# Optimization experiments

Measured on AMD Instinct MI355X. Metric: run time of the kernel, lower is better.

Reference implementation:

```python
import jax, jax.numpy as jnp
import numpy as np

N_VERTICES = 1_000_000
N_EDGES = 16_000_000


def setup_inputs() -> dict:
    key = jax.random.key(0)
    k1, k2, k3, k4 = jax.random.split(key, 4)
    # vertex_attr columns: [A_ii, b_i, x_i]; keep A_ii away from 0 for stable division
    A_ii = jax.random.uniform(k1, (N_VERTICES,), jnp.float32, 1.0, 2.0)
    b_i = jax.random.normal(k2, (N_VERTICES,), jnp.float32)
    x_i = jnp.zeros((N_VERTICES,), jnp.float32)
    vertex_attr = jnp.stack([A_ii, b_i, x_i], axis=1)  # [N, 3]
    # edge_attr columns: [A_ij, c_ij] (c_ij is overwritten on first iteration)
    A_ij = jax.random.normal(k3, (N_EDGES,), jnp.float32) * 0.01
    edge_attr = jnp.stack([A_ij, jnp.zeros_like(A_ij)], axis=1)  # [E, 2]
    edgeij_pair = jax.random.randint(k4, (2, N_EDGES), 0, N_VERTICES, jnp.int64)
    g = jnp.array([0.666], jnp.float32)  # Jacobi damping weight w
    return {"n_iters": 10, "vertex_attr": vertex_attr, "edgeij_pair": edgeij_pair,
            "edge_attr": edge_attr, "g": g}


def reference(n_iters, vertex_attr, edgeij_pair, edge_attr, g):
    # MetaLayer convention: row, col = edge_index; vattr_j = x[col]; scatter to row.
    row = edgeij_pair[0]
    col = edgeij_pair[1]
    A_ii = vertex_attr[:, 0]          # [N]
    b_i = vertex_attr[:, 1]           # [N]
    x0 = vertex_attr[:, 2]            # [N]
    A_ij = edge_attr[:, 0]            # [E]
    w = g[0]
    n = A_ii.shape[0]

    def step(x, _):
        # EdgeUpdate: c_ij = A_ij * x_j ; aggregation: cbar_i = sum_j c_ij
        c_ij = A_ij * x[col]                                     # [E]
        cbar = jax.ops.segment_sum(c_ij, row, num_segments=n)    # [N]
        # VertexUpdate: x <- x + w * (b - cbar) / A_ii
        x_new = x + w * (b_i - cbar) / A_ii
        return x_new, None

    x, _ = jax.lax.scan(step, x0, None, length=n_iters)
    return x.reshape(-1, 1)
```

## Files before the change

kernel.cpp:

```cpp
#include <hip/hip_runtime.h>
#include <hip/hip_fp16.h>

static constexpr int BLK  = 256;
static constexpr int B1   = 256;
static constexpr int BLKW = 1024;

__global__ void detect_kernel(const unsigned long long* __restrict__ rc,
                              int* __restrict__ flag) {
    if (blockIdx.x == 0 && threadIdx.x == 0) {
        int is64 = 1;
        for (int i = 0; i < 8; ++i)
            if (rc[i] >= (1ull << 20)) is64 = 0;
        *flag = is64;
    }
}

__global__ void hist1_kernel(const void* __restrict__ rcv,
                             const int* __restrict__ flag,
                             unsigned int* __restrict__ hist, int ne, int nb) {
    __shared__ unsigned int lh[1024];
    const int b = blockIdx.x;
    const int chunk = (ne + B1 - 1) / B1;
    const int s = b * chunk, e = min(ne, s + chunk);
    for (int i = threadIdx.x; i < 1024; i += BLKW) lh[i] = 0u;
    __syncthreads();
    const int is64 = *flag;
    const unsigned long long* r64 = (const unsigned long long*)rcv;
    const unsigned int*       r32 = (const unsigned int*)rcv;
    for (int i = s + threadIdx.x; i < e; i += BLKW) {
        unsigned int row = is64 ? (unsigned int)r64[i] : r32[i];
        atomicAdd(&lh[row >> 10], 1u);
    }
    __syncthreads();
    for (int i = threadIdx.x; i < nb; i += BLKW)
        hist[(size_t)i * B1 + b] = lh[i];
}

__global__ void scan1_kernel(unsigned int* __restrict__ data,
                             unsigned int* __restrict__ part, int n) {
    __shared__ unsigned int s[BLK];
    int t = threadIdx.x;
    int i = blockIdx.x * BLK + t;
    unsigned int v = (i < n) ? data[i] : 0u;
    s[t] = v;
    __syncthreads();
    for (int off = 1; off < BLK; off <<= 1) {
        unsigned int u = (t >= off) ? s[t - off] : 0u;
        __syncthreads();
        s[t] += u;
        __syncthreads();
    }
    if (i < n) data[i] = s[t] - v;
    if (t == BLK - 1) part[blockIdx.x] = s[t];
}

__global__ void scan2_kernel(unsigned int* __restrict__ part, int np) {
    __shared__ unsigned int s[BLK];
    __shared__ unsigned int carry_s;
    int t = threadIdx.x;
    if (t == 0) carry_s = 0u;
    __syncthreads();
    for (int base = 0; base < np; base += BLK) {
        int i = base + t;
        unsigned int v = (i < np) ? part[i] : 0u;
        s[t] = v;
        __syncthreads();
        for (int off = 1; off < BLK; off <<= 1) {
            unsigned int u = (t >= off) ? s[t - off] : 0u;
            __syncthreads();
            s[t] += u;
            __syncthreads();
        }
        unsigned int carry = carry_s;
        if (i < np) part[i] = s[t] - v + carry;
        __syncthreads();
        if (t == BLK - 1) carry_s = carry + s[t];
        __syncthreads();
    }
}

__global__ void scan3_kernel(unsigned int* __restrict__ data,
                             const unsigned int* __restrict__ part, int n) {
    int i = blockIdx.x * BLK + threadIdx.x;
    if (i < n) data[i] += part[blockIdx.x];
}

__global__ void scatter1_kernel(const void* __restrict__ rcv,
                                const float2* __restrict__ eattr,
                                const int* __restrict__ flag,
                                const unsigned int* __restrict__ base,
                                unsigned long long* __restrict__ edges,
                                int ne, int nb) {
    __shared__ unsigned int cur[1024];
    const int b = blockIdx.x;
    const int chunk = (ne + B1 - 1) / B1;
    const int s = b * chunk, e = min(ne, s + chunk);
    for (int i = threadIdx.x; i < nb; i += BLKW)
        cur[i] = base[(size_t)i * B1 + b];
    __syncthreads();
    const int is64 = *flag;
    const unsigned long long* r64 = (const unsigned long long*)rcv;
    const unsigned int*       r32 = (const unsigned int*)rcv;
    for (int i = s + threadIdx.x; i < e; i += BLKW) {
        unsigned long long row, col;
        if (is64) { row = r64[i]; col = r64[(size_t)ne + i]; }
        else      { row = r32[i]; col = r32[(size_t)ne + i]; }
        float a = eattr[i].x;
        unsigned short h = __half_as_ushort(__float2half(a));
        unsigned long long q = (row << 44) | (col << 24) | (unsigned long long)h;
        unsigned int pos = atomicAdd(&cur[(unsigned int)(row >> 10)], 1u);
        edges[pos] = q;
    }
}

__global__ void vprep_kernel(const float* __restrict__ vattr,
                             const float* __restrict__ g,
                             float2* __restrict__ vp,
                             float* __restrict__ x0, int nv) {
    int i = blockIdx.x * BLK + threadIdx.x;
    if (i >= nv) return;
    float A = vattr[3 * i + 0];
    float b = vattr[3 * i + 1];
    float x = vattr[3 * i + 2];
    float w = g[0];
    vp[i] = make_float2(w * b / A, w / A);
    x0[i] = x;
}

__global__ void iter_kernel(const unsigned int* __restrict__ bbase,
                            const unsigned long long* __restrict__ edges,
                            const float2* __restrict__ vp,
                            const float* __restrict__ xin,
                            float* __restrict__ xout,
                            int nv, int ne, int nb) {
    __shared__ float acc[1024];
    const int b = blockIdx.x;
    const int t = threadIdx.x;
    for (int i = t; i < 1024; i += BLK) acc[i] = 0.0f;
    __syncthreads();
    const unsigned int s = bbase[(size_t)b * B1];
    const unsigned int e = (b == nb - 1) ? (unsigned int)ne
                                         : bbase[(size_t)(b + 1) * B1];
    #pragma unroll 4
    for (unsigned int j = s + t; j < e; j += BLK) {
        unsigned long long q = edges[j];
        float a = __half2float(__ushort_as_half((unsigned short)(q & 0xFFFFu)));
        unsigned int col = (unsigned int)(q >> 24) & 0xFFFFFu;
        unsigned int rlo = (unsigned int)(q >> 44) & 1023u;
        atomicAdd(&acc[rlo], a * xin[col]);
    }
    __syncthreads();
    const int r0 = b << 10;
    for (int i = t; i < 1024; i += BLK) {
        int r = r0 + i;
        if (r < nv) {
            float2 qv = vp[r];
            xout[r] = xin[r] + qv.x - qv.y * acc[i];
        }
    }
}

extern "C" void kernel_launch(void* const* d_in, const int* in_sizes, int n_in,
                              void* d_out, int out_size, void* d_ws, size_t ws_size,
                              hipStream_t stream) {
    const float* vattr = (const float*)d_in[1];
    const void*  eij   = (const void*)d_in[2];
    const float* eattr = (const float*)d_in[3];
    const float* g     = (const float*)d_in[4];
    const int nv = in_sizes[1] / 3;
    const int ne = in_sizes[3] / 2;
    const int n_iters = 10;
    const int nb = (nv + 1023) >> 10;
    const int nh = nb * B1;

    char* ws = (char*)d_ws;
    size_t off = 0;
    auto alloc = [&](size_t bytes) -> void* {
        void* p = ws + off;
        off = (off + bytes + 255) & ~(size_t)255;
        return p;
    };
    unsigned long long* edges = (unsigned long long*)alloc((size_t)ne * 8);
    unsigned int* hist = (unsigned int*)alloc((size_t)nh * 4);
    unsigned int* part = (unsigned int*)alloc(((size_t)(nh + BLK - 1) / BLK) * 4);
    float2* vp = (float2*)alloc((size_t)nv * 8);
    float*  xa = (float*) alloc((size_t)nv * 4);
    float*  xb = (float*) alloc((size_t)nv * 4);
    int*  flag = (int*)   alloc(256);

    const int vblocks = (nv + BLK - 1) / BLK;
    const int sblocks = (nh + BLK - 1) / BLK;

    detect_kernel<<<1, 64, 0, stream>>>((const unsigned long long*)eij, flag);
    hist1_kernel<<<B1, BLKW, 0, stream>>>(eij, flag, hist, ne, nb);
    scan1_kernel<<<sblocks, BLK, 0, stream>>>(hist, part, nh);
    scan2_kernel<<<1, BLK, 0, stream>>>(part, sblocks);
    scan3_kernel<<<sblocks, BLK, 0, stream>>>(hist, part, nh);
    scatter1_kernel<<<B1, BLKW, 0, stream>>>(eij, (const float2*)eattr, flag,
                                             hist, edges, ne, nb);
    vprep_kernel<<<vblocks, BLK, 0, stream>>>(vattr, g, vp, xa, nv);

    float* xin  = xa;
    float* xout = xb;
    for (int it = 0; it < n_iters; ++it) {
        float* dst = (it == n_iters - 1) ? (float*)d_out : xout;
        iter_kernel<<<nb, BLK, 0, stream>>>(hist, edges, vp, xin, dst,
                                            nv, ne, nb);
        float* t = xin; xin = dst; xout = t;
    }
}
```

Measured before the change: 1.406 ms.

## Halve row-bucket size, unroll edge loop by 8 with nontemporal loads

```diff
diff --git a/kernel.cpp b/kernel.cpp
--- a/kernel.cpp
+++ b/kernel.cpp
@@ -4,6 +4,9 @@
 static constexpr int BLK  = 256;
 static constexpr int B1   = 256;
 static constexpr int BLKW = 1024;
+static constexpr int RSH  = 9;
+static constexpr int RMSK = 511;
+static constexpr int NBMAX = 2048;
 
 __global__ void detect_kernel(const unsigned long long* __restrict__ rc,
                               int* __restrict__ flag) {
@@ -18,18 +21,18 @@
 __global__ void hist1_kernel(const void* __restrict__ rcv,
                              const int* __restrict__ flag,
                              unsigned int* __restrict__ hist, int ne, int nb) {
-    __shared__ unsigned int lh[1024];
+    __shared__ unsigned int lh[NBMAX];
     const int b = blockIdx.x;
     const int chunk = (ne + B1 - 1) / B1;
     const int s = b * chunk, e = min(ne, s + chunk);
-    for (int i = threadIdx.x; i < 1024; i += BLKW) lh[i] = 0u;
+    for (int i = threadIdx.x; i < NBMAX; i += BLKW) lh[i] = 0u;
     __syncthreads();
     const int is64 = *flag;
     const unsigned long long* r64 = (const unsigned long long*)rcv;
     const unsigned int*       r32 = (const unsigned int*)rcv;
     for (int i = s + threadIdx.x; i < e; i += BLKW) {
         unsigned int row = is64 ? (unsigned int)r64[i] : r32[i];
-        atomicAdd(&lh[row >> 10], 1u);
+        atomicAdd(&lh[row >> RSH], 1u);
     }
     __syncthreads();
     for (int i = threadIdx.x; i < nb; i += BLKW)
@@ -91,7 +94,7 @@
                                 const unsigned int* __restrict__ base,
                                 unsigned long long* __restrict__ edges,
                                 int ne, int nb) {
-    __shared__ unsigned int cur[1024];
+    __shared__ unsigned int cur[NBMAX];
     const int b = blockIdx.x;
     const int chunk = (ne + B1 - 1) / B1;
     const int s = b * chunk, e = min(ne, s + chunk);
@@ -108,7 +111,7 @@
         float a = eattr[i].x;
         unsigned short h = __half_as_ushort(__float2half(a));
         unsigned long long q = (row << 44) | (col << 24) | (unsigned long long)h;
-        unsigned int pos = atomicAdd(&cur[(unsigned int)(row >> 10)], 1u);
+        unsigned int pos = atomicAdd(&cur[(unsigned int)(row >> RSH)], 1u);
         edges[pos] = q;
     }
 }
@@ -127,35 +130,59 @@
     x0[i] = x;
 }
 
+__device__ __forceinline__ void edge_accum(unsigned long long q,
+                                           const float* __restrict__ xin,
+                                           float* acc) {
+    float a = __half2float(__ushort_as_half((unsigned short)(q & 0xFFFFu)));
+    unsigned int col = (unsigned int)(q >> 24) & 0xFFFFFu;
+    unsigned int rlo = (unsigned int)(q >> 44) & RMSK;
+    atomicAdd(&acc[rlo], a * xin[col]);
+}
+
 __global__ void iter_kernel(const unsigned int* __restrict__ bbase,
                             const unsigned long long* __restrict__ edges,
                             const float2* __restrict__ vp,
                             const float* __restrict__ xin,
                             float* __restrict__ xout,
                             int nv, int ne, int nb) {
-    __shared__ float acc[1024];
+    __shared__ float acc[512];
     const int b = blockIdx.x;
     const int t = threadIdx.x;
-    for (int i = t; i < 1024; i += BLK) acc[i] = 0.0f;
+    for (int i = t; i < 512; i += BLK) acc[i] = 0.0f;
     __syncthreads();
     const unsigned int s = bbase[(size_t)b * B1];
     const unsigned int e = (b == nb - 1) ? (unsigned int)ne
                                          : bbase[(size_t)(b + 1) * B1];
-    #pragma unroll 4
-    for (unsigned int j = s + t; j < e; j += BLK) {
-        unsigned long long q = edges[j];
-        float a = __half2float(__ushort_as_half((unsigned short)(q & 0xFFFFu)));
-        unsigned int col = (unsigned int)(q >> 24) & 0xFFFFFu;
-        unsigned int rlo = (unsigned int)(q >> 44) & 1023u;
-        atomicAdd(&acc[rlo], a * xin[col]);
-    }
-    __syncthreads();
-    const int r0 = b << 10;
-    for (int i = t; i < 1024; i += BLK) {
+    unsigned int j = s + t;
+    for (; j + 7u * BLK < e; j += 8u * BLK) {
+        unsigned long long q0 = __builtin_nontemporal_load(&edges[j + 0u * BLK]);
+        unsigned long long q1 = __builtin_nontemporal_load(&edges[j + 1u * BLK]);
+        unsigned long long q2 = __builtin_nontemporal_load(&edges[j + 2u * BLK]);
+        unsigned long long q3 = __builtin_nontemporal_load(&edges[j + 3u * BLK]);
+        unsigned long long q4 = __builtin_nontemporal_load(&edges[j + 4u * BLK]);
+        unsigned long long q5 = __builtin_nontemporal_load(&edges[j + 5u * BLK]);
+        unsigned long long q6 = __builtin_nontemporal_load(&edges[j + 6u * BLK]);
+        unsigned long long q7 = __builtin_nontemporal_load(&edges[j + 7u * BLK]);
+        edge_accum(q0, xin, acc);
+        edge_accum(q1, xin, acc);
+        edge_accum(q2, xin, acc);
+        edge_accum(q3, xin, acc);
+        edge_accum(q4, xin, acc);
+        edge_accum(q5, xin, acc);
+        edge_accum(q6, xin, acc);
+        edge_accum(q7, xin, acc);
+    }
+    for (; j < e; j += BLK) {
+        unsigned long long q = __builtin_nontemporal_load(&edges[j]);
+        edge_accum(q, xin, acc);
+    }
+    __syncthreads();
+    const int r0 = b << RSH;
+    for (int i = t; i < 512; i += BLK) {
         int r = r0 + i;
         if (r < nv) {
             float2 qv = vp[r];
-            xout[r] = xin[r] + qv.x - qv.y * acc[i];
+            __builtin_nontemporal_store(xin[r] + qv.x - qv.y * acc[i], &xout[r]);
         }
     }
 }
@@ -170,7 +197,7 @@
     const int nv = in_sizes[1] / 3;
     const int ne = in_sizes[3] / 2;
     const int n_iters = 10;
-    const int nb = (nv + 1023) >> 10;
+    const int nb = (nv + RMSK) >> RSH;
     const int nh = nb * B1;
 
     char* ws = (char*)d_ws;
```

New measurement: 1.512 ms. +7.6%, slower.

## Sort edges by column within larger row buckets and split accumulation

Applied to the files above, without the earlier changes.

```diff
diff --git a/kernel.cpp b/kernel.cpp
--- a/kernel.cpp
+++ b/kernel.cpp
@@ -4,9 +4,14 @@
 static constexpr int BLK  = 256;
 static constexpr int B1   = 256;
 static constexpr int BLKW = 1024;
-
-__global__ void detect_kernel(const unsigned long long* __restrict__ rc,
-                              int* __restrict__ flag) {
+static constexpr int RSH  = 13;
+static constexpr int RPB  = 8192;
+static constexpr int RMSK = 8191;
+static constexpr int NBMAX = 128;
+
+typedef unsigned long long ull;
+
+__global__ void detect_kernel(const ull* __restrict__ rc, int* __restrict__ flag) {
     if (blockIdx.x == 0 && threadIdx.x == 0) {
         int is64 = 1;
         for (int i = 0; i < 8; ++i)
@@ -18,18 +23,18 @@
 __global__ void hist1_kernel(const void* __restrict__ rcv,
                              const int* __restrict__ flag,
                              unsigned int* __restrict__ hist, int ne, int nb) {
-    __shared__ unsigned int lh[1024];
+    __shared__ unsigned int lh[NBMAX];
     const int b = blockIdx.x;
     const int chunk = (ne + B1 - 1) / B1;
     const int s = b * chunk, e = min(ne, s + chunk);
-    for (int i = threadIdx.x; i < 1024; i += BLKW) lh[i] = 0u;
+    for (int i = threadIdx.x; i < NBMAX; i += BLKW) lh[i] = 0u;
     __syncthreads();
     const int is64 = *flag;
-    const unsigned long long* r64 = (const unsigned long long*)rcv;
-    const unsigned int*       r32 = (const unsigned int*)rcv;
+    const ull*          r64 = (const ull*)rcv;
+    const unsigned int* r32 = (const unsigned int*)rcv;
     for (int i = s + threadIdx.x; i < e; i += BLKW) {
         unsigned int row = is64 ? (unsigned int)r64[i] : r32[i];
-        atomicAdd(&lh[row >> 10], 1u);
+        atomicAdd(&lh[row >> RSH], 1u);
     }
     __syncthreads();
     for (int i = threadIdx.x; i < nb; i += BLKW)
@@ -89,9 +94,8 @@
                                 const float2* __restrict__ eattr,
                                 const int* __restrict__ flag,
                                 const unsigned int* __restrict__ base,
-                                unsigned long long* __restrict__ edges,
-                                int ne, int nb) {
-    __shared__ unsigned int cur[1024];
+                                ull* __restrict__ edges, int ne, int nb) {
+    __shared__ unsigned int cur[NBMAX];
     const int b = blockIdx.x;
     const int chunk = (ne + B1 - 1) / B1;
     const int s = b * chunk, e = min(ne, s + chunk);
@@ -99,17 +103,53 @@
         cur[i] = base[(size_t)i * B1 + b];
     __syncthreads();
     const int is64 = *flag;
-    const unsigned long long* r64 = (const unsigned long long*)rcv;
-    const unsigned int*       r32 = (const unsigned int*)rcv;
+    const ull*          r64 = (const ull*)rcv;
+    const unsigned int* r32 = (const unsigned int*)rcv;
     for (int i = s + threadIdx.x; i < e; i += BLKW) {
-        unsigned long long row, col;
+        ull row, col;
         if (is64) { row = r64[i]; col = r64[(size_t)ne + i]; }
         else      { row = r32[i]; col = r32[(size_t)ne + i]; }
         float a = eattr[i].x;
         unsigned short h = __half_as_ushort(__float2half(a));
-        unsigned long long q = (row << 44) | (col << 24) | (unsigned long long)h;
-        unsigned int pos = atomicAdd(&cur[(unsigned int)(row >> 10)], 1u);
+        ull q = (row << 44) | (col << 24) | (ull)h;
+        unsigned int pos = atomicAdd(&cur[(unsigned int)(row >> RSH)], 1u);
         edges[pos] = q;
+    }
+}
+
+__global__ void colsort_kernel(const ull* __restrict__ edges,
+                               const unsigned int* __restrict__ base,
+                               ull* __restrict__ edges2,
+                               unsigned int* __restrict__ mid, int ne, int nb) {
+    __shared__ unsigned int bins[1024];
+    __shared__ unsigned int cur[1024];
+    const int b = blockIdx.x;
+    const int t = threadIdx.x;
+    const unsigned int s = base[(size_t)b * B1];
+    const unsigned int e = (b == nb - 1) ? (unsigned int)ne
+                                         : base[(size_t)(b + 1) * B1];
+    bins[t] = 0u;
+    __syncthreads();
+    for (unsigned int j = s + t; j < e; j += BLKW) {
+        ull q = edges[j];
+        atomicAdd(&bins[(unsigned int)(q >> 34) & 1023u], 1u);
+    }
+    __syncthreads();
+    unsigned int v = bins[t];
+    for (int off = 1; off < 1024; off <<= 1) {
+        unsigned int u = (t >= off) ? bins[t - off] : 0u;
+        __syncthreads();
+        bins[t] += u;
+        __syncthreads();
+    }
+    unsigned int excl = bins[t] - v;
+    cur[t] = excl;
+    if (t == 512) mid[b] = s + excl;
+    __syncthreads();
+    for (unsigned int j = s + t; j < e; j += BLKW) {
+        ull q = edges[j];
+        unsigned int pos = atomicAdd(&cur[(unsigned int)(q >> 34) & 1023u], 1u);
+        edges2[s + pos] = q;
     }
 }
 
@@ -127,37 +167,51 @@
     x0[i] = x;
 }
 
-__global__ void iter_kernel(const unsigned int* __restrict__ bbase,
-                            const unsigned long long* __restrict__ edges,
-                            const float2* __restrict__ vp,
-                            const float* __restrict__ xin,
-                            float* __restrict__ xout,
-                            int nv, int ne, int nb) {
-    __shared__ float acc[1024];
-    const int b = blockIdx.x;
+__global__ __launch_bounds__(BLKW)
+void iter_kernel(const unsigned int* __restrict__ base,
+                 const unsigned int* __restrict__ mid,
+                 const ull* __restrict__ edges2,
+                 const float* __restrict__ xin,
+                 float* __restrict__ p0, float* __restrict__ p1,
+                 int ne, int nb) {
+    __shared__ float acc[RPB];
+    const int blk = blockIdx.x;
+    const int b = blk >> 1, half = blk & 1;
     const int t = threadIdx.x;
-    for (int i = t; i < 1024; i += BLK) acc[i] = 0.0f;
-    __syncthreads();
-    const unsigned int s = bbase[(size_t)b * B1];
-    const unsigned int e = (b == nb - 1) ? (unsigned int)ne
-                                         : bbase[(size_t)(b + 1) * B1];
+    #pragma unroll
+    for (int i = t; i < RPB; i += BLKW) acc[i] = 0.0f;
+    __syncthreads();
+    const unsigned int s0 = base[(size_t)b * B1];
+    const unsigned int e0 = (b == nb - 1) ? (unsigned int)ne
+                                          : base[(size_t)(b + 1) * B1];
+    const unsigned int m = mid[b];
+    const unsigned int s = half ? m : s0;
+    const unsigned int e = half ? e0 : m;
     #pragma unroll 4
-    for (unsigned int j = s + t; j < e; j += BLK) {
-        unsigned long long q = edges[j];
+    for (unsigned int j = s + t; j < e; j += BLKW) {
+        ull q = edges2[j];
         float a = __half2float(__ushort_as_half((unsigned short)(q & 0xFFFFu)));
         unsigned int col = (unsigned int)(q >> 24) & 0xFFFFFu;
-        unsigned int rlo = (unsigned int)(q >> 44) & 1023u;
-        atomicAdd(&acc[rlo], a * xin[col]);
-    }
-    __syncthreads();
-    const int r0 = b << 10;
-    for (int i = t; i < 1024; i += BLK) {
-        int r = r0 + i;
-        if (r < nv) {
-            float2 qv = vp[r];
-            xout[r] = xin[r] + qv.x - qv.y * acc[i];
-        }
-    }
+        unsigned int r   = (unsigned int)(q >> 44) & RMSK;
+        atomicAdd(&acc[r], a * xin[col]);
+    }
+    __syncthreads();
+    float* p = half ? p1 : p0;
+    const size_t r0 = (size_t)b << RSH;
+    #pragma unroll
+    for (int i = t; i < RPB; i += BLKW) p[r0 + i] = acc[i];
+}
+
+__global__ void merge_kernel(const float* __restrict__ p0,
+                             const float* __restrict__ p1,
+                             const float2* __restrict__ vp,
+                             const float* __restrict__ xin,
+                             float* __restrict__ xout, int nv) {
+    int i = blockIdx.x * BLK + threadIdx.x;
+    if (i >= nv) return;
+    float c = p0[i] + p1[i];
+    float2 q = vp[i];
+    xout[i] = xin[i] + q.x - q.y * c;
 }
 
 extern "C" void kernel_launch(void* const* d_in, const int* in_sizes, int n_in,
@@ -170,8 +224,9 @@
     const int nv = in_sizes[1] / 3;
     const int ne = in_sizes[3] / 2;
     const int n_iters = 10;
-    const int nb = (nv + 1023) >> 10;
+    const int nb = (nv + RMSK) >> RSH;
     const int nh = nb * B1;
+    const int nprows = nb << RSH;
 
     char* ws = (char*)d_ws;
     size_t off = 0;
@@ -180,9 +235,13 @@
         off = (off + bytes + 255) & ~(size_t)255;
         return p;
     };
-    unsigned long long* edges = (unsigned long long*)alloc((size_t)ne * 8);
+    ull* edges  = (ull*)alloc((size_t)ne * 8);
+    ull* edges2 = (ull*)alloc((size_t)ne * 8);
     unsigned int* hist = (unsigned int*)alloc((size_t)nh * 4);
     unsigned int* part = (unsigned int*)alloc(((size_t)(nh + BLK - 1) / BLK) * 4);
+    unsigned int* mid  = (unsigned int*)alloc((size_t)nb * 4);
+    float* p0 = (float*)alloc((size_t)nprows * 4);
+    float* p1 = (float*)alloc((size_t)nprows * 4);
     float2* vp = (float2*)alloc((size_t)nv * 8);
     float*  xa = (float*) alloc((size_t)nv * 4);
     float*  xb = (float*) alloc((size_t)nv * 4);
@@ -191,21 +250,23 @@
     const int vblocks = (nv + BLK - 1) / BLK;
     const int sblocks = (nh + BLK - 1) / BLK;
 
-    detect_kernel<<<1, 64, 0, stream>>>((const unsigned long long*)eij, flag);
+    detect_kernel<<<1, 64, 0, stream>>>((const ull*)eij, flag);
     hist1_kernel<<<B1, BLKW, 0, stream>>>(eij, flag, hist, ne, nb);
     scan1_kernel<<<sblocks, BLK, 0, stream>>>(hist, part, nh);
     scan2_kernel<<<1, BLK, 0, stream>>>(part, sblocks);
     scan3_kernel<<<sblocks, BLK, 0, stream>>>(hist, part, nh);
     scatter1_kernel<<<B1, BLKW, 0, stream>>>(eij, (const float2*)eattr, flag,
                                              hist, edges, ne, nb);
+    colsort_kernel<<<nb, BLKW, 0, stream>>>(edges, hist, edges2, mid, ne, nb);
     vprep_kernel<<<vblocks, BLK, 0, stream>>>(vattr, g, vp, xa, nv);
 
     float* xin  = xa;
     float* xout = xb;
     for (int it = 0; it < n_iters; ++it) {
+        iter_kernel<<<2 * nb, BLKW, 0, stream>>>(hist, mid, edges2, xin,
+                                                 p0, p1, ne, nb);
         float* dst = (it == n_iters - 1) ? (float*)d_out : xout;
-        iter_kernel<<<nb, BLK, 0, stream>>>(hist, edges, vp, xin, dst,
-                                            nv, ne, nb);
+        merge_kernel<<<vblocks, BLK, 0, stream>>>(p0, p1, vp, xin, dst, nv);
         float* t = xin; xin = dst; xout = t;
     }
 }
```

New measurement: 1.447 ms. +3.0%, slower.

## Partition edges by row block and column range with per-plane partial sums

Applied to the files above, without the earlier changes.

```diff
diff --git a/kernel.cpp b/kernel.cpp
--- a/kernel.cpp
+++ b/kernel.cpp
@@ -4,9 +4,16 @@
 static constexpr int BLK  = 256;
 static constexpr int B1   = 256;
 static constexpr int BLKW = 1024;
-
-__global__ void detect_kernel(const unsigned long long* __restrict__ rc,
-                              int* __restrict__ flag) {
+static constexpr int RSH  = 14;
+static constexpr int RPB  = 16384;
+static constexpr int RMSK = 16383;
+static constexpr int NCS  = 4;
+static constexpr int CSH  = 18;
+static constexpr int NSMAX = 256;
+
+typedef unsigned long long ull;
+
+__global__ void detect_kernel(const ull* __restrict__ rc, int* __restrict__ flag) {
     if (blockIdx.x == 0 && threadIdx.x == 0) {
         int is64 = 1;
         for (int i = 0; i < 8; ++i)
@@ -17,22 +24,25 @@
 
 __global__ void hist1_kernel(const void* __restrict__ rcv,
                              const int* __restrict__ flag,
-                             unsigned int* __restrict__ hist, int ne, int nb) {
-    __shared__ unsigned int lh[1024];
+                             unsigned int* __restrict__ hist, int ne, int nseg) {
+    __shared__ unsigned int lh[NSMAX];
     const int b = blockIdx.x;
     const int chunk = (ne + B1 - 1) / B1;
     const int s = b * chunk, e = min(ne, s + chunk);
-    for (int i = threadIdx.x; i < 1024; i += BLKW) lh[i] = 0u;
+    for (int i = threadIdx.x; i < NSMAX; i += BLKW) lh[i] = 0u;
     __syncthreads();
     const int is64 = *flag;
-    const unsigned long long* r64 = (const unsigned long long*)rcv;
-    const unsigned int*       r32 = (const unsigned int*)rcv;
+    const ull*          r64 = (const ull*)rcv;
+    const unsigned int* r32 = (const unsigned int*)rcv;
     for (int i = s + threadIdx.x; i < e; i += BLKW) {
-        unsigned int row = is64 ? (unsigned int)r64[i] : r32[i];
-        atomicAdd(&lh[row >> 10], 1u);
-    }
-    __syncthreads();
-    for (int i = threadIdx.x; i < nb; i += BLKW)
+        unsigned int row, col;
+        if (is64) { row = (unsigned int)r64[i]; col = (unsigned int)r64[(size_t)ne + i]; }
+        else      { row = r32[i];               col = r32[(size_t)ne + i]; }
+        unsigned int seg = (row >> RSH) * NCS + (col >> CSH);
+        atomicAdd(&lh[seg], 1u);
+    }
+    __syncthreads();
+    for (int i = threadIdx.x; i < nseg; i += BLKW)
         hist[(size_t)i * B1 + b] = lh[i];
 }
 
@@ -89,26 +99,27 @@
                                 const float2* __restrict__ eattr,
                                 const int* __restrict__ flag,
                                 const unsigned int* __restrict__ base,
-                                unsigned long long* __restrict__ edges,
-                                int ne, int nb) {
-    __shared__ unsigned int cur[1024];
+                                ull* __restrict__ edges, int ne, int nseg) {
+    __shared__ unsigned int cur[NSMAX];
     const int b = blockIdx.x;
     const int chunk = (ne + B1 - 1) / B1;
     const int s = b * chunk, e = min(ne, s + chunk);
-    for (int i = threadIdx.x; i < nb; i += BLKW)
+    for (int i = threadIdx.x; i < nseg; i += BLKW)
         cur[i] = base[(size_t)i * B1 + b];
     __syncthreads();
     const int is64 = *flag;
-    const unsigned long long* r64 = (const unsigned long long*)rcv;
-    const unsigned int*       r32 = (const unsigned int*)rcv;
+    const ull*          r64 = (const ull*)rcv;
+    const unsigned int* r32 = (const unsigned int*)rcv;
     for (int i = s + threadIdx.x; i < e; i += BLKW) {
-        unsigned long long row, col;
+        ull row, col;
         if (is64) { row = r64[i]; col = r64[(size_t)ne + i]; }
         else      { row = r32[i]; col = r32[(size_t)ne + i]; }
         float a = eattr[i].x;
         unsigned short h = __half_as_ushort(__float2half(a));
-        unsigned long long q = (row << 44) | (col << 24) | (unsigned long long)h;
-        unsigned int pos = atomicAdd(&cur[(unsigned int)(row >> 10)], 1u);
+        ull q = (row << 44) | (col << 24) | (ull)h;
+        unsigned int seg = (unsigned int)(row >> RSH) * NCS
+                         + (unsigned int)(col >> CSH);
+        unsigned int pos = atomicAdd(&cur[seg], 1u);
         edges[pos] = q;
     }
 }
@@ -127,37 +138,46 @@
     x0[i] = x;
 }
 
-__global__ void iter_kernel(const unsigned int* __restrict__ bbase,
-                            const unsigned long long* __restrict__ edges,
-                            const float2* __restrict__ vp,
-                            const float* __restrict__ xin,
-                            float* __restrict__ xout,
-                            int nv, int ne, int nb) {
-    __shared__ float acc[1024];
-    const int b = blockIdx.x;
+__global__ __launch_bounds__(BLKW)
+void iter_kernel(const unsigned int* __restrict__ base,
+                 const ull* __restrict__ edges,
+                 const float* __restrict__ xin,
+                 float* __restrict__ p,
+                 int ne, int nseg, int nprows) {
+    __shared__ float acc[RPB];
+    const int i = blockIdx.x;
+    const int b = i >> 2, cs = i & 3;
     const int t = threadIdx.x;
-    for (int i = t; i < 1024; i += BLK) acc[i] = 0.0f;
-    __syncthreads();
-    const unsigned int s = bbase[(size_t)b * B1];
-    const unsigned int e = (b == nb - 1) ? (unsigned int)ne
-                                         : bbase[(size_t)(b + 1) * B1];
+    #pragma unroll
+    for (int k = t; k < RPB; k += BLKW) acc[k] = 0.0f;
+    __syncthreads();
+    const unsigned int s = base[(size_t)i * B1];
+    const unsigned int e = (i == nseg - 1) ? (unsigned int)ne
+                                           : base[(size_t)(i + 1) * B1];
     #pragma unroll 4
-    for (unsigned int j = s + t; j < e; j += BLK) {
-        unsigned long long q = edges[j];
+    for (unsigned int j = s + t; j < e; j += BLKW) {
+        ull q = edges[j];
         float a = __half2float(__ushort_as_half((unsigned short)(q & 0xFFFFu)));
         unsigned int col = (unsigned int)(q >> 24) & 0xFFFFFu;
-        unsigned int rlo = (unsigned int)(q >> 44) & 1023u;
-        atomicAdd(&acc[rlo], a * xin[col]);
-    }
-    __syncthreads();
-    const int r0 = b << 10;
-    for (int i = t; i < 1024; i += BLK) {
-        int r = r0 + i;
-        if (r < nv) {
-            float2 qv = vp[r];
-            xout[r] = xin[r] + qv.x - qv.y * acc[i];
-        }
-    }
+        unsigned int r   = (unsigned int)(q >> 44) & RMSK;
+        atomicAdd(&acc[r], a * xin[col]);
+    }
+    __syncthreads();
+    float* plane = p + (size_t)cs * nprows + ((size_t)b << RSH);
+    #pragma unroll
+    for (int k = t; k < RPB; k += BLKW) plane[k] = acc[k];
+}
+
+__global__ void merge_kernel(const float* __restrict__ p,
+                             const float2* __restrict__ vp,
+                             const float* __restrict__ xin,
+                             float* __restrict__ xout, int nv, int nprows) {
+    int i = blockIdx.x * BLK + threadIdx.x;
+    if (i >= nv) return;
+    float c = p[i] + p[(size_t)nprows + i]
+            + p[2 * (size_t)nprows + i] + p[3 * (size_t)nprows + i];
+    float2 q = vp[i];
+    xout[i] = xin[i] + q.x - q.y * c;
 }
 
 extern "C" void kernel_launch(void* const* d_in, const int* in_sizes, int n_in,
@@ -170,8 +190,10 @@
     const int nv = in_sizes[1] / 3;
     const int ne = in_sizes[3] / 2;
     const int n_iters = 10;
-    const int nb = (nv + 1023) >> 10;
-    const int nh = nb * B1;
+    const int nb   = (nv + RMSK) >> RSH;
+    const int nseg = nb * NCS;
+    const int nh   = nseg * B1;
+    const int nprows = nb << RSH;
 
     char* ws = (char*)d_ws;
     size_t off = 0;
@@ -180,9 +202,10 @@
         off = (off + bytes + 255) & ~(size_t)255;
         return p;
     };
-    unsigned long long* edges = (unsigned long long*)alloc((size_t)ne * 8);
+    ull* edges = (ull*)alloc((size_t)ne * 8);
     unsigned int* hist = (unsigned int*)alloc((size_t)nh * 4);
     unsigned int* part = (unsigned int*)alloc(((size_t)(nh + BLK - 1) / BLK) * 4);
+    float* p = (float*)alloc((size_t)NCS * nprows * 4);
     float2* vp = (float2*)alloc((size_t)nv * 8);
     float*  xa = (float*) alloc((size_t)nv * 4);
     float*  xb = (float*) alloc((size_t)nv * 4);
@@ -191,21 +214,22 @@
     const int vblocks = (nv + BLK - 1) / BLK;
     const int sblocks = (nh + BLK - 1) / BLK;
 
-    detect_kernel<<<1, 64, 0, stream>>>((const unsigned long long*)eij, flag);
-    hist1_kernel<<<B1, BLKW, 0, stream>>>(eij, flag, hist, ne, nb);
+    detect_kernel<<<1, 64, 0, stream>>>((const ull*)eij, flag);
+    hist1_kernel<<<B1, BLKW, 0, stream>>>(eij, flag, hist, ne, nseg);
     scan1_kernel<<<sblocks, BLK, 0, stream>>>(hist, part, nh);
     scan2_kernel<<<1, BLK, 0, stream>>>(part, sblocks);
     scan3_kernel<<<sblocks, BLK, 0, stream>>>(hist, part, nh);
     scatter1_kernel<<<B1, BLKW, 0, stream>>>(eij, (const float2*)eattr, flag,
-                                             hist, edges, ne, nb);
+                                             hist, edges, ne, nseg);
     vprep_kernel<<<vblocks, BLK, 0, stream>>>(vattr, g, vp, xa, nv);
 
     float* xin  = xa;
     float* xout = xb;
     for (int it = 0; it < n_iters; ++it) {
+        iter_kernel<<<nseg, BLKW, 0, stream>>>(hist, edges, xin, p, ne, nseg,
+                                               nprows);
         float* dst = (it == n_iters - 1) ? (float*)d_out : xout;
-        iter_kernel<<<nb, BLK, 0, stream>>>(hist, edges, vp, xin, dst,
-                                            nv, ne, nb);
+        merge_kernel<<<vblocks, BLK, 0, stream>>>(p, vp, xin, dst, nv, nprows);
         float* t = xin; xin = dst; xout = t;
     }
 }
```

Measured after the change: 1.248 ms. 11.2% less time.
